# Optimization experiments

Measured on AMD Instinct MI355X. Metric: run time of the kernel, lower is better.

Reference implementation:

```python
import jax, jax.numpy as jnp
import numpy as np

D = 1024
H = 16
DH = D // H  # 64

def setup_inputs() -> dict:
    key = jax.random.key(0)
    ks = jax.random.split(key, 9)
    B, L = 2, 2048
    s = 1.0 / np.sqrt(D)
    inp = {
        'x':  jax.random.normal(ks[0], (B, L, D), dtype=jnp.float32),
        'Wq': jax.random.uniform(ks[1], (D, D), jnp.float32, -s, s),
        'bq': jnp.zeros((D,), jnp.float32),
        'Wk': jax.random.uniform(ks[2], (D, D), jnp.float32, -s, s),
        'bk': jnp.zeros((D,), jnp.float32),
        'Wv': jax.random.uniform(ks[3], (D, D), jnp.float32, -s, s),
        'bv': jnp.zeros((D,), jnp.float32),
        'Wo': jax.random.uniform(ks[4], (D, D), jnp.float32, -s, s),
        'bo': jnp.zeros((D,), jnp.float32),
    }
    return inp

def reference(x, Wq, bq, Wk, bk, Wv, bv, Wo, bo):
    B, L, _ = x.shape
    # projections (torch Linear: x @ W.T + b; here weights stored as [D_in, D_out])
    q = (x @ Wq + bq).reshape(B, L, H, DH).transpose(0, 2, 1, 3)  # [B,H,L,DH]
    k = (x @ Wk + bk).reshape(B, L, H, DH).transpose(0, 2, 1, 3)
    v = (x @ Wv + bv).reshape(B, L, H, DH).transpose(0, 2, 1, 3)
    scores = jnp.einsum('bhqd,bhkd->bhqk', q, k) / jnp.sqrt(jnp.float32(DH))
    attn = jax.nn.softmax(scores, axis=-1)  # dropout p=0 / eval -> identity
    out = jnp.einsum('bhqk,bhkd->bhqd', attn, v)
    out = out.transpose(0, 2, 1, 3).reshape(B, L, D)
    return out @ Wo + bo
```

## Files before the change

kernel.cpp:

```cpp
#include <hip/hip_runtime.h>
#include <stdint.h>

typedef __attribute__((ext_vector_type(8)))  __bf16 bf16x8;
typedef __attribute__((ext_vector_type(4)))  __bf16 bf16x4;
typedef __attribute__((ext_vector_type(4)))  float  f32x4;
typedef __attribute__((ext_vector_type(16))) float  f32x16;
typedef __attribute__((ext_vector_type(4)))  int    i32x4;

#define DEV static __device__ __forceinline__

DEV float fast_exp2(float x) {
#if __has_builtin(__builtin_amdgcn_exp2f)
  return __builtin_amdgcn_exp2f(x);
#else
  return exp2f(x);
#endif
}

DEV uint32_t pack_bf2(float a, float b) {
  __bf16 x = (__bf16)a, y = (__bf16)b;
  uint16_t xu = __builtin_bit_cast(uint16_t, x);
  uint16_t yu = __builtin_bit_cast(uint16_t, y);
  return (uint32_t)xu | ((uint32_t)yu << 16);
}

DEV void gload_lds16(const void* g, void* l) {
  __builtin_amdgcn_global_load_lds(
      (const __attribute__((address_space(1))) void*)(uintptr_t)(g),
      (__attribute__((address_space(3))) void*)(uint32_t)(uintptr_t)(l),
      16, 0, 0);
}

#define SM_SCALE 0.18033688f

__global__ void k_prep(const float* __restrict__ x,  __bf16* __restrict__ xb,
                       const float* __restrict__ Wq, const float* __restrict__ Wk,
                       const float* __restrict__ Wv, const float* __restrict__ Wo,
                       __bf16* __restrict__ wtq, __bf16* __restrict__ wot) {
  const int z = blockIdx.z;
  if (z < 4) {
    const float* W  = (z == 0) ? Wq : (z == 1) ? Wk : (z == 2) ? Wv : Wo;
    __bf16*      Wt = (z == 3) ? wot : (wtq + (size_t)z * 1024 * 1024);
    __shared__ __bf16 T[64][66];
    int t = threadIdx.x;
    int r = t >> 2;
    int cq = (t & 3) << 4;
    {
      int gk = blockIdx.y * 64 + r;
      int gn0 = blockIdx.x * 64 + cq;
      const float* src = W + (size_t)gk * 1024 + gn0;
#pragma unroll
      for (int j = 0; j < 16; j += 4) {
        f32x4 v = *(const f32x4*)(src + j);
#pragma unroll
        for (int jj = 0; jj < 4; ++jj) T[r][cq + j + jj] = (__bf16)v[jj];
      }
    }
    __syncthreads();
    {
      int gn = blockIdx.x * 64 + r;
      int gk0 = blockIdx.y * 64 + cq;
      __bf16* dst = Wt + (size_t)gn * 1024 + gk0;
      bf16x8 o0, o1;
#pragma unroll
      for (int j = 0; j < 8; ++j) { o0[j] = T[cq + j][r]; o1[j] = T[cq + 8 + j][r]; }
      *(bf16x8*)dst = o0;
      *(bf16x8*)(dst + 8) = o1;
    }
  } else {
    int lb = (z - 4) * 256 + blockIdx.y * 16 + blockIdx.x;
    int i = (lb * 256 + (int)threadIdx.x) * 4;
    if (i < 4096 * 1024) {
      f32x4 v = *(const f32x4*)(x + i);
      bf16x4 o;
      o[0] = (__bf16)v[0]; o[1] = (__bf16)v[1];
      o[2] = (__bf16)v[2]; o[3] = (__bf16)v[3];
      *(bf16x4*)(xb + i) = o;
    }
  }
}

__global__ void k_vt(const __bf16* __restrict__ qkv, __bf16* __restrict__ kvf) {
  int lt = blockIdx.x, bh = blockIdx.y, z = blockIdx.z;
  int b = bh >> 4, h = bh & 15;
  int t = threadIdx.x;
  int lane = t & 63, slot = t >> 6;
  int l31 = lane & 31, hi = lane >> 5;

  if (z == 1) {
#pragma unroll
    for (int tt = 0; tt < 2; ++tt) {
      const __bf16* src = qkv + (size_t)(b * 2048 + lt * 64 + tt * 32 + l31) * 3072
                          + 1024 + h * 64 + slot * 16 + hi * 8;
      __bf16* dst = kvf + (size_t)(bh * 64 + lt * 2 + tt) * 4096 + slot * 512 + lane * 8;
      *(bf16x8*)dst = *(const bf16x8*)src;
    }
    return;
  }

  __shared__ __bf16 T[64][66];
  {
    int r = t >> 2, cq = (t & 3) << 4;
    const __bf16* src = qkv + (size_t)(b * 2048 + lt * 64 + r) * 3072 + 2048 + h * 64 + cq;
    bf16x8 v0 = *(const bf16x8*)src;
    bf16x8 v1 = *(const bf16x8*)(src + 8);
#pragma unroll
    for (int j = 0; j < 8; ++j) { T[r][cq + j] = v0[j]; T[r][cq + 8 + j] = v1[j]; }
  }
  __syncthreads();
#pragma unroll
  for (int tt = 0; tt < 2; ++tt) {
    bf16x8 val;
#pragma unroll
    for (int j = 0; j < 8; ++j)
      val[j] = T[tt * 32 + ((slot >> 1) * 2 + hi) * 8 + j][(slot & 1) * 32 + l31];
    __bf16* dst = kvf + (size_t)(bh * 64 + lt * 2 + tt) * 4096 + 2048 + slot * 512 + lane * 8;
    *(bf16x8*)dst = val;
  }
}

__global__ void k_gemm0(const __bf16* __restrict__ A, const __bf16* __restrict__ Bt,
                        __bf16* __restrict__ Cout, int M, int N, int K,
                        const float* __restrict__ b0, const float* __restrict__ b1,
                        const float* __restrict__ b2) {
  __shared__ __align__(16) __bf16 As[128 * 64];
  __shared__ __align__(16) __bf16 Bs[128 * 64];
  const int t = threadIdx.x, wid = t >> 6, lane = t & 63;
  const int bm = blockIdx.y, bn = blockIdx.x;
  const int wm = wid >> 1, wn = wid & 1;
  const int l15 = lane & 15, l4 = lane >> 4;
  const int rr = lane >> 3, cc = lane & 7;
  f32x4 acc[4][4] = {};
  const int nk = K >> 6;
  for (int kt = 0; kt < nk; ++kt) {
    __syncthreads();
#pragma unroll
    for (int j = 0; j < 4; ++j) {
      int row = wid * 32 + j * 8 + rr;
      int csrc = (cc ^ (row & 7)) * 8;
      gload_lds16(A + (size_t)(bm * 128 + row) * K + kt * 64 + csrc,
                  (char*)As + (wid * 32 + j * 8) * 128);
      gload_lds16(Bt + (size_t)(bn * 128 + row) * K + kt * 64 + csrc,
                  (char*)Bs + (wid * 32 + j * 8) * 128);
    }
    __syncthreads();
#pragma unroll
    for (int kk = 0; kk < 2; ++kk) {
      bf16x8 a[4], b[4];
#pragma unroll
      for (int ms = 0; ms < 4; ++ms) {
        int row = wm * 64 + ms * 16 + l15;
        a[ms] = *(const bf16x8*)((char*)As + row * 128 + (((kk * 4 + l4) ^ (row & 7)) * 16));
      }
#pragma unroll
      for (int ns = 0; ns < 4; ++ns) {
        int row = wn * 64 + ns * 16 + l15;
        b[ns] = *(const bf16x8*)((char*)Bs + row * 128 + (((kk * 4 + l4) ^ (row & 7)) * 16));
      }
#pragma unroll
      for (int ms = 0; ms < 4; ++ms)
#pragma unroll
        for (int ns = 0; ns < 4; ++ns)
          acc[ms][ns] = __builtin_amdgcn_mfma_f32_16x16x32_bf16(a[ms], b[ns], acc[ms][ns], 0, 0, 0);
    }
  }
#pragma unroll
  for (int ms = 0; ms < 4; ++ms) {
#pragma unroll
    for (int ns = 0; ns < 4; ++ns) {
      int n = bn * 128 + wn * 64 + ns * 16 + l15;
      const float* bp = (n < 1024) ? b0 : ((n < 2048) ? b1 : b2);
      float bias = bp[n & 1023];
#pragma unroll
      for (int i = 0; i < 4; ++i) {
        int m = bm * 128 + wm * 64 + ms * 16 + l4 * 4 + i;
        float v = acc[ms][ns][i] + bias;
        if (n < 1024) v *= SM_SCALE;
        Cout[(size_t)m * N + n] = (__bf16)v;
      }
    }
  }
}

__global__ void k_gemm64(const __bf16* __restrict__ A, const __bf16* __restrict__ Bt,
                         float* __restrict__ Cout, int M, int N, int K,
                         const float* __restrict__ b0) {
  __shared__ __align__(16) __bf16 As[64 * 64];
  __shared__ __align__(16) __bf16 Bs[64 * 64];
  const int t = threadIdx.x, wid = t >> 6, lane = t & 63;
  const int bm = blockIdx.y, bn = blockIdx.x;
  const int wm = wid >> 1, wn = wid & 1;
  const int l15 = lane & 15, l4 = lane >> 4;
  const int rr = lane >> 3, cc = lane & 7;
  f32x4 acc[2][2] = {};
  const int nk = K >> 6;
  for (int kt = 0; kt < nk; ++kt) {
    __syncthreads();
#pragma unroll
    for (int j = 0; j < 2; ++j) {
      int row = wid * 16 + j * 8 + rr;
      int csrc = (cc ^ (row & 7)) * 8;
      gload_lds16(A + (size_t)(bm * 64 + row) * K + kt * 64 + csrc,
                  (char*)As + (wid * 16 + j * 8) * 128);
      gload_lds16(Bt + (size_t)(bn * 64 + row) * K + kt * 64 + csrc,
                  (char*)Bs + (wid * 16 + j * 8) * 128);
    }
    __syncthreads();
#pragma unroll
    for (int kk = 0; kk < 2; ++kk) {
      bf16x8 a[2], b[2];
#pragma unroll
      for (int ms = 0; ms < 2; ++ms) {
        int row = wm * 32 + ms * 16 + l15;
        a[ms] = *(const bf16x8*)((char*)As + row * 128 + (((kk * 4 + l4) ^ (row & 7)) * 16));
      }
#pragma unroll
      for (int ns = 0; ns < 2; ++ns) {
        int row = wn * 32 + ns * 16 + l15;
        b[ns] = *(const bf16x8*)((char*)Bs + row * 128 + (((kk * 4 + l4) ^ (row & 7)) * 16));
      }
#pragma unroll
      for (int ms = 0; ms < 2; ++ms)
#pragma unroll
        for (int ns = 0; ns < 2; ++ns)
          acc[ms][ns] = __builtin_amdgcn_mfma_f32_16x16x32_bf16(a[ms], b[ns], acc[ms][ns], 0, 0, 0);
    }
  }
#pragma unroll
  for (int ms = 0; ms < 2; ++ms) {
#pragma unroll
    for (int ns = 0; ns < 2; ++ns) {
      int n = bn * 64 + wn * 32 + ns * 16 + l15;
      float bias = b0[n];
#pragma unroll
      for (int i = 0; i < 4; ++i) {
        int m = bm * 64 + wm * 32 + ms * 16 + l4 * 4 + i;
        Cout[(size_t)m * N + n] = acc[ms][ns][i] + bias;
      }
    }
  }
}

__global__ void __launch_bounds__(256, 3)
k_attn(const __bf16* __restrict__ qkv, const __bf16* __restrict__ kvf,
       __bf16* __restrict__ Aout) {
  __shared__ __align__(16) char smem[16896];
  const int t = threadIdx.x, w = t >> 6, lane = t & 63;
  const int qsub = w & 1, half = w >> 1;
  const int l31 = lane & 31, hi = lane >> 5;
  const int f = blockIdx.x;
  const int qt = (f >> 3) & 31;
  const int bh = (f & 7) + 8 * (f >> 8);
  const int b = bh >> 4, h = bh & 15;

  const char* kvbase = (const char*)kvf + (size_t)(bh * 64 + half * 32) * 8192 + lane * 16;

  bf16x8 aq[4];
  {
    int qrow = b * 2048 + qt * 64 + qsub * 32 + l31;
    const __bf16* qp = qkv + (size_t)qrow * 3072 + h * 64 + hi * 8;
#pragma unroll
    for (int d = 0; d < 4; ++d) aq[d] = *(const bf16x8*)(qp + d * 16);
  }

  f32x16 o[2] = {};
  float lsum = 0.f;

  bf16x8 kA[4], vA[4], kB[4], vB[4];

  auto LOAD = [&](bf16x8* kf, bf16x8* vf, int tl) {
    const char* p = kvbase + (size_t)tl * 8192;
#pragma unroll
    for (int i = 0; i < 4; ++i) kf[i] = *(const bf16x8*)(p + i * 1024);
#pragma unroll
    for (int i = 0; i < 4; ++i) vf[i] = *(const bf16x8*)(p + 4096 + i * 1024);
  };

  auto BODY = [&](const bf16x8* kf, const bf16x8* vf) {
    f32x16 s;
    s = 0.f;
    __builtin_amdgcn_s_setprio(1);
#pragma unroll
    for (int d = 0; d < 4; ++d)
      s = __builtin_amdgcn_mfma_f32_32x32x16_bf16(kf[d], aq[d], s, 0, 0, 0);
    __builtin_amdgcn_s_setprio(0);

#pragma unroll
    for (int r = 0; r < 16; ++r) s[r] = fast_exp2(s[r]);

    float u[8];
#pragma unroll
    for (int c = 0; c < 8; ++c) u[c] = s[2 * c] + s[2 * c + 1];
#pragma unroll
    for (int st = 4; st > 0; st >>= 1)
#pragma unroll
      for (int c = 0; c < st; ++c) u[c] += u[c + st];
    lsum += u[0];

    uint32_t W[8];
#pragma unroll
    for (int c = 0; c < 8; ++c) W[c] = pack_bf2(s[2 * c], s[2 * c + 1]);

    bf16x8 pa[2];
#pragma unroll
    for (int kstep = 0; kstep < 2; ++kstep) {
      const int base = 4 * kstep;
      uint32_t w0 = W[base + 0], w1 = W[base + 1];
      uint32_t w2 = W[base + 2], w3 = W[base + 3];
      uint32_t x0 = __shfl_xor((int)w0, 32);
      uint32_t x1 = __shfl_xor((int)w1, 32);
      uint32_t x2 = __shfl_xor((int)w2, 32);
      uint32_t x3 = __shfl_xor((int)w3, 32);
      i32x4 pw;
      pw[0] = (int)(hi ? x2 : w0);
      pw[1] = (int)(hi ? x3 : w1);
      pw[2] = (int)(hi ? w2 : x0);
      pw[3] = (int)(hi ? w3 : x1);
      pa[kstep] = __builtin_bit_cast(bf16x8, pw);
    }

    __builtin_amdgcn_s_setprio(1);
#pragma unroll
    for (int kstep = 0; kstep < 2; ++kstep)
#pragma unroll
      for (int db = 0; db < 2; ++db)
        o[db] = __builtin_amdgcn_mfma_f32_32x32x16_bf16(pa[kstep], vf[kstep * 2 + db], o[db], 0, 0, 0);
    __builtin_amdgcn_s_setprio(0);
  };

  LOAD(kA, vA, 0);
  for (int tl = 0; tl < 32; tl += 2) {
    LOAD(kB, vB, tl + 1);
    BODY(kA, vA);
    if (tl + 2 < 32) LOAD(kA, vA, tl + 2);
    BODY(kB, vB);
  }

  lsum += __shfl_xor(lsum, 32);

  float* oLDS = (float*)smem;
  float* sLDS = (float*)(smem + 16384);
  if (half == 1) {
    float* ob = oLDS + qsub * 2048;
#pragma unroll
    for (int db = 0; db < 2; ++db)
#pragma unroll
      for (int r = 0; r < 16; ++r)
        ob[(db * 16 + r) * 64 + lane] = o[db][r];
    sLDS[qsub * 64 + lane] = lsum;
  }
  __syncthreads();
  if (half == 0) {
    const float* ob = oLDS + qsub * 2048;
#pragma unroll
    for (int db = 0; db < 2; ++db)
#pragma unroll
      for (int r = 0; r < 16; ++r)
        o[db][r] += ob[(db * 16 + r) * 64 + lane];
    lsum += sLDS[qsub * 64 + lane];

#pragma unroll
    for (int r = 0; r < 16; ++r) {
      int rowq = (r & 3) + 8 * (r >> 2) + 4 * hi;
      float inv = 1.0f / __shfl(lsum, rowq);
      int qg = b * 2048 + qt * 64 + qsub * 32 + rowq;
#pragma unroll
      for (int db = 0; db < 2; ++db) {
        int col = h * 64 + db * 32 + l31;
        Aout[(size_t)qg * 1024 + col] = (__bf16)(o[db][r] * inv);
      }
    }
  }
}

extern "C" void kernel_launch(void* const* d_in, const int* in_sizes, int n_in,
                              void* d_out, int out_size, void* d_ws, size_t ws_size,
                              hipStream_t stream) {
  const float* x  = (const float*)d_in[0];
  const float* Wq = (const float*)d_in[1];
  const float* bq = (const float*)d_in[2];
  const float* Wk = (const float*)d_in[3];
  const float* bk = (const float*)d_in[4];
  const float* Wv = (const float*)d_in[5];
  const float* bv = (const float*)d_in[6];
  const float* Wo = (const float*)d_in[7];
  const float* bo = (const float*)d_in[8];
  float* out = (float*)d_out;

  char* ws = (char*)d_ws;
  __bf16* xb   = (__bf16*)(ws);
  __bf16* aout = (__bf16*)(ws);
  __bf16* wtq  = (__bf16*)(ws + (8ull  << 20));
  __bf16* wot  = (__bf16*)(ws + (14ull << 20));
  __bf16* qkv  = (__bf16*)(ws + (16ull << 20));
  __bf16* kvf  = (__bf16*)(ws + (40ull << 20));

  k_prep<<<dim3(16, 16, 20), 256, 0, stream>>>(x, xb, Wq, Wk, Wv, Wo, wtq, wot);

  k_gemm0<<<dim3(24, 32), 256, 0, stream>>>(xb, wtq, qkv, 4096, 3072, 1024, bq, bk, bv);

  k_vt<<<dim3(32, 32, 2), 256, 0, stream>>>(qkv, kvf);

  k_attn<<<dim3(1024), 256, 0, stream>>>(qkv, kvf, aout);

  k_gemm64<<<dim3(16, 64), 256, 0, stream>>>(aout, wot, out, 4096, 1024, 1024, bo);
}
```

Before: 114.6 us.

## Process two query sub-tiles per wave to reuse loaded K/V fragments

Each attention wave now holds two 32-row query fragments and runs the QK/softmax/PV body twice per loaded K/V tile, so a block covers 128 queries and the grid is halved. This halves global K/V fragment loads per query and gives more independent MFMA work to hide latency. In exchange register pressure roughly doubles (launch bounds drop to 2 blocks/SM), LDS for the cross-half reduction doubles, and there are fewer blocks to fill the GPU.

```diff
diff --git a/kernel.cpp b/kernel.cpp
--- a/kernel.cpp
+++ b/kernel.cpp
@@ -241,30 +241,33 @@
   }
 }
 
-__global__ void __launch_bounds__(256, 3)
+__global__ void __launch_bounds__(256, 2)
 k_attn(const __bf16* __restrict__ qkv, const __bf16* __restrict__ kvf,
        __bf16* __restrict__ Aout) {
-  __shared__ __align__(16) char smem[16896];
+  __shared__ __align__(16) char smem[33792];
   const int t = threadIdx.x, w = t >> 6, lane = t & 63;
-  const int qsub = w & 1, half = w >> 1;
+  const int qpair = w & 1, half = w >> 1;
   const int l31 = lane & 31, hi = lane >> 5;
   const int f = blockIdx.x;
-  const int qt = (f >> 3) & 31;
-  const int bh = (f & 7) + 8 * (f >> 8);
+  const int qt = (f >> 3) & 15;
+  const int bh = (f & 7) + 8 * (f >> 7);
   const int b = bh >> 4, h = bh & 15;
 
   const char* kvbase = (const char*)kvf + (size_t)(bh * 64 + half * 32) * 8192 + lane * 16;
 
-  bf16x8 aq[4];
+  bf16x8 aqA[4], aqB[4];
   {
-    int qrow = b * 2048 + qt * 64 + qsub * 32 + l31;
+    int qrow = b * 2048 + qt * 128 + qpair * 64 + l31;
     const __bf16* qp = qkv + (size_t)qrow * 3072 + h * 64 + hi * 8;
 #pragma unroll
-    for (int d = 0; d < 4; ++d) aq[d] = *(const bf16x8*)(qp + d * 16);
-  }
-
-  f32x16 o[2] = {};
-  float lsum = 0.f;
+    for (int d = 0; d < 4; ++d) aqA[d] = *(const bf16x8*)(qp + d * 16);
+    qp += (size_t)32 * 3072;
+#pragma unroll
+    for (int d = 0; d < 4; ++d) aqB[d] = *(const bf16x8*)(qp + d * 16);
+  }
+
+  f32x16 oA[2] = {}, oB[2] = {};
+  float lsA = 0.f, lsB = 0.f;
 
   bf16x8 kA[4], vA[4], kB[4], vB[4];
 
@@ -276,7 +279,8 @@
     for (int i = 0; i < 4; ++i) vf[i] = *(const bf16x8*)(p + 4096 + i * 1024);
   };
 
-  auto BODY = [&](const bf16x8* kf, const bf16x8* vf) {
+  auto BODY = [&](const bf16x8* kf, const bf16x8* vf, const bf16x8* aq,
+                  f32x16* o, float& lsum) {
     f32x16 s;
     s = 0.f;
     __builtin_amdgcn_s_setprio(1);
@@ -331,43 +335,56 @@
   LOAD(kA, vA, 0);
   for (int tl = 0; tl < 32; tl += 2) {
     LOAD(kB, vB, tl + 1);
-    BODY(kA, vA);
+    BODY(kA, vA, aqA, oA, lsA);
+    BODY(kA, vA, aqB, oB, lsB);
     if (tl + 2 < 32) LOAD(kA, vA, tl + 2);
-    BODY(kB, vB);
-  }
-
-  lsum += __shfl_xor(lsum, 32);
+    BODY(kB, vB, aqA, oA, lsA);
+    BODY(kB, vB, aqB, oB, lsB);
+  }
+
+  lsA += __shfl_xor(lsA, 32);
+  lsB += __shfl_xor(lsB, 32);
 
   float* oLDS = (float*)smem;
-  float* sLDS = (float*)(smem + 16384);
+  float* sLDS = (float*)(smem + 32768);
   if (half == 1) {
-    float* ob = oLDS + qsub * 2048;
+    float* obA = oLDS + (qpair * 2 + 0) * 2048;
+    float* obB = oLDS + (qpair * 2 + 1) * 2048;
 #pragma unroll
     for (int db = 0; db < 2; ++db)
 #pragma unroll
-      for (int r = 0; r < 16; ++r)
-        ob[(db * 16 + r) * 64 + lane] = o[db][r];
-    sLDS[qsub * 64 + lane] = lsum;
+      for (int r = 0; r < 16; ++r) {
+        obA[(db * 16 + r) * 64 + lane] = oA[db][r];
+        obB[(db * 16 + r) * 64 + lane] = oB[db][r];
+      }
+    sLDS[(qpair * 2 + 0) * 64 + lane] = lsA;
+    sLDS[(qpair * 2 + 1) * 64 + lane] = lsB;
   }
   __syncthreads();
   if (half == 0) {
-    const float* ob = oLDS + qsub * 2048;
+    const float* obA = oLDS + (qpair * 2 + 0) * 2048;
+    const float* obB = oLDS + (qpair * 2 + 1) * 2048;
 #pragma unroll
     for (int db = 0; db < 2; ++db)
 #pragma unroll
-      for (int r = 0; r < 16; ++r)
-        o[db][r] += ob[(db * 16 + r) * 64 + lane];
-    lsum += sLDS[qsub * 64 + lane];
-
+      for (int r = 0; r < 16; ++r) {
+        oA[db][r] += obA[(db * 16 + r) * 64 + lane];
+        oB[db][r] += obB[(db * 16 + r) * 64 + lane];
+      }
+    lsA += sLDS[(qpair * 2 + 0) * 64 + lane];
+    lsB += sLDS[(qpair * 2 + 1) * 64 + lane];
+
+    int qbase = b * 2048 + qt * 128 + qpair * 64;
 #pragma unroll
     for (int r = 0; r < 16; ++r) {
       int rowq = (r & 3) + 8 * (r >> 2) + 4 * hi;
-      float inv = 1.0f / __shfl(lsum, rowq);
-      int qg = b * 2048 + qt * 64 + qsub * 32 + rowq;
+      float invA = 1.0f / __shfl(lsA, rowq);
+      float invB = 1.0f / __shfl(lsB, rowq);
 #pragma unroll
       for (int db = 0; db < 2; ++db) {
         int col = h * 64 + db * 32 + l31;
-        Aout[(size_t)qg * 1024 + col] = (__bf16)(o[db][r] * inv);
+        Aout[(size_t)(qbase + rowq) * 1024 + col]      = (__bf16)(oA[db][r] * invA);
+        Aout[(size_t)(qbase + 32 + rowq) * 1024 + col] = (__bf16)(oB[db][r] * invB);
       }
     }
   }
@@ -401,7 +418,7 @@
 
   k_vt<<<dim3(32, 32, 2), 256, 0, stream>>>(qkv, kvf);
 
-  k_attn<<<dim3(1024), 256, 0, stream>>>(qkv, kvf, aout);
+  k_attn<<<dim3(512), 256, 0, stream>>>(qkv, kvf, aout);
 
   k_gemm64<<<dim3(16, 64), 256, 0, stream>>>(aout, wot, out, 4096, 1024, 1024, bo);
 }
```

Result: faster. 110.3 us (-3.7%).
